# Optimization experiments

Measured on AMD Instinct MI355X. Metric: run time of the kernel, lower is better.

## Reference

```python
import jax, jax.numpy as jnp
import numpy as np

N_IN, N_HID, N_OUT = 2048, 4096, 1024
N_TOT = N_IN + N_HID + N_OUT
BATCH = 4096


def _structure_mask():
    # input -> {hidden, output}; hidden -> {hidden, output}; nothing feeds inputs,
    # outputs feed nothing.
    m = np.zeros((N_TOT, N_TOT), dtype=np.float32)
    m[0:N_IN, N_IN:N_TOT] = 1.0
    m[N_IN:N_IN + N_HID, N_IN:N_TOT] = 1.0
    return jnp.asarray(m)


def setup_inputs() -> dict:
    key = jax.random.key(0)
    kx, kw = jax.random.split(key)
    x = jax.random.normal(kx, (BATCH, N_IN), dtype=jnp.float32)
    weights = jax.random.normal(kw, (N_TOT, N_TOT), dtype=jnp.float32) * 0.1
    structure_mask = _structure_mask()
    return {"x": x, "weights": weights, "structure_mask": structure_mask}


def reference(x, weights, structure_mask):
    # Faithful to the torch forward: the per-neuron hidden loop reads the
    # activation vector BEFORE any hidden value is written, so every hidden
    # unit sees only [x, 0, 0]; outputs then see [x, hidden, 0].
    Wm = weights * structure_mask  # (N_TOT, N_TOT)
    B = x.shape[0]
    a0 = jnp.concatenate(
        [x, jnp.zeros((B, N_HID + N_OUT), dtype=x.dtype)], axis=1)  # (B, N_TOT)
    hidden = jax.nn.relu(a0 @ Wm[:, N_IN:N_IN + N_HID])             # (B, N_HID)
    a1 = jnp.concatenate(
        [x, hidden, jnp.zeros((B, N_OUT), dtype=x.dtype)], axis=1)  # (B, N_TOT)
    out = a1 @ Wm[:, N_IN + N_HID:]                                 # (B, N_OUT)
    return out
```

## Files before the change

kernel.cpp:

```cpp
#include <hip/hip_runtime.h>
#include <hip/hip_bf16.h>

#define N_IN  2048
#define N_HID 4096
#define N_OUT 1024
#define N_TOT 7168
#define BATCH 4096
#define LDA2  (N_IN + N_HID)
#define OUT_ELEMS ((size_t)BATCH * N_OUT)

typedef __attribute__((ext_vector_type(8))) short short8;
typedef __attribute__((ext_vector_type(4))) float f32x4;

static __device__ __forceinline__ unsigned short f2bf(float f) {
  __hip_bfloat16 h = __float2bfloat16(f);
  return __builtin_bit_cast(unsigned short, h);
}

__global__ void conv_x_kernel(const float* __restrict__ x,
                              unsigned short* __restrict__ A2) {
  int idx = blockIdx.x * 256 + threadIdx.x;
  int row = idx >> 9;
  int col = (idx & 511) << 2;
  const float4 v = *(const float4*)(x + (size_t)row * N_IN + col);
  ushort4 o;
  o.x = f2bf(v.x); o.y = f2bf(v.y); o.z = f2bf(v.z); o.w = f2bf(v.w);
  *(ushort4*)(A2 + (size_t)row * LDA2 + col) = o;
}

__global__ void conv_t_kernel(const float* __restrict__ src, int lds_,
                              unsigned short* __restrict__ dst, int ldd) {
  __shared__ float tile[32][33];
  const int t = threadIdx.x;
  const int k0 = blockIdx.y << 5, n0 = blockIdx.x << 5;
  const int r = t >> 3, c = (t & 7) << 2;
  const float4 v = *(const float4*)(src + (size_t)(k0 + r) * lds_ + n0 + c);
  tile[r][c] = v.x; tile[r][c + 1] = v.y; tile[r][c + 2] = v.z; tile[r][c + 3] = v.w;
  __syncthreads();
  ushort4 o;
  o.x = f2bf(tile[c][r]);
  o.y = f2bf(tile[c + 1][r]);
  o.z = f2bf(tile[c + 2][r]);
  o.w = f2bf(tile[c + 3][r]);
  *(ushort4*)(dst + (size_t)(n0 + r) * ldd + k0 + c) = o;
}

__global__ void add3_kernel(const float* __restrict__ P, float* __restrict__ out) {
  size_t i = ((size_t)blockIdx.x * 256 + threadIdx.x) * 4;
  float4 a = *(const float4*)(P + i);
  float4 b = *(const float4*)(P + OUT_ELEMS + i);
  float4 c = *(const float4*)(P + 2 * OUT_ELEMS + i);
  float4 o;
  o.x = (a.x + b.x) + c.x;
  o.y = (a.y + b.y) + c.y;
  o.z = (a.z + b.z) + c.z;
  o.w = (a.w + b.w) + c.w;
  *(float4*)(out + i) = o;
}

struct GemmCtx {
  int lane, wave, wy, wx, lm, quad;
  int grow, gcol;
};

static __device__ __forceinline__ void gemm_kloop(
    const unsigned short* __restrict__ Ag, int lda,
    const unsigned short* __restrict__ Bg, int ldb,
    unsigned short* As, unsigned short* Bs, const GemmCtx& cx,
    int Klen, f32x4 acc[4][4]) {
  unsigned short* Asl = As + cx.wave * 2048;
  unsigned short* Bsl = Bs + cx.wave * 2048;
  for (int ko = 0; ko < Klen; ko += 64) {
    __syncthreads();
#pragma unroll
    for (int i = 0; i < 4; ++i) {
      __builtin_amdgcn_global_load_lds(
          (const __attribute__((address_space(1))) void*)(Ag + (size_t)(8 * i) * lda + ko),
          (__attribute__((address_space(3))) void*)(Asl + i * 512), 16, 0, 0);
      __builtin_amdgcn_global_load_lds(
          (const __attribute__((address_space(1))) void*)(Bg + (size_t)(8 * i) * ldb + ko),
          (__attribute__((address_space(3))) void*)(Bsl + i * 512), 16, 0, 0);
    }
    __syncthreads();

#pragma unroll
    for (int kk = 0; kk < 2; ++kk) {
      short8 av[4], bv[4];
#pragma unroll
      for (int mt = 0; mt < 4; ++mt) {
        const int r = cx.wy * 64 + mt * 16 + cx.lm;
        av[mt] = *(const short8*)(As + r * 64 + (((kk * 4 + cx.quad) ^ (cx.lm & 7)) << 3));
      }
#pragma unroll
      for (int nt = 0; nt < 4; ++nt) {
        const int r = cx.wx * 64 + nt * 16 + cx.lm;
        bv[nt] = *(const short8*)(Bs + r * 64 + (((kk * 4 + cx.quad) ^ (cx.lm & 7)) << 3));
      }
#pragma unroll
      for (int mt = 0; mt < 4; ++mt)
#pragma unroll
        for (int nt = 0; nt < 4; ++nt)
          acc[mt][nt] = __builtin_amdgcn_mfma_f32_16x16x32_bf16(
              av[mt], bv[nt], acc[mt][nt], 0, 0, 0);
    }
  }
}

static __device__ __forceinline__ void epilogue_f32(
    char* smem, const GemmCtx& cx, f32x4 acc[4][4],
    float* __restrict__ C, int ldc, int row_base, int col_base, int tid) {
  float* Csf = (float*)smem;
#pragma unroll
  for (int p = 0; p < 2; ++p) {
    if (cx.wy == p) {
#pragma unroll
      for (int mt = 0; mt < 4; ++mt) {
        const int row0 = mt * 16 + cx.quad * 4;
#pragma unroll
        for (int nt = 0; nt < 4; ++nt) {
          const int col = cx.wx * 64 + nt * 16 + cx.lm;
#pragma unroll
          for (int r = 0; r < 4; ++r)
            Csf[(row0 + r) * 132 + col] = acc[mt][nt][r];
        }
      }
    }
    __syncthreads();
    const int col = (tid & 31) << 2;
#pragma unroll
    for (int i = 0; i < 8; ++i) {
      const int row = (tid >> 5) + 8 * i;
      float4 v = *(const float4*)(Csf + row * 132 + col);
      *(float4*)(C + (size_t)(row_base + p * 64 + row) * ldc + col_base + col) = v;
    }
    if (p == 0) __syncthreads();
  }
}

__global__ __launch_bounds__(256)
void gemm_fused(const unsigned short* __restrict__ A, int lda,
                const unsigned short* __restrict__ Bt, int ldb,
                unsigned short* __restrict__ Hout,
                float* __restrict__ P0) {
  __shared__ __align__(16) char smem[34816];
  unsigned short* As = (unsigned short*)smem;
  unsigned short* Bs = (unsigned short*)(smem + 16384);

  const int tid = threadIdx.x;
  GemmCtx cx;
  cx.lane = tid & 63; cx.wave = tid >> 6;
  cx.wy = cx.wave >> 1; cx.wx = cx.wave & 1;
  cx.lm = cx.lane & 15; cx.quad = cx.lane >> 4;
  cx.grow = (cx.wave << 5) + (cx.lane >> 3);
  cx.gcol = ((cx.lane & 7) ^ (cx.lane >> 3)) << 3;
  const int bm = blockIdx.y, bn = blockIdx.x;

  const unsigned short* Ag = A  + (size_t)(bm * 128 + cx.grow) * lda + cx.gcol;
  const unsigned short* Bg = Bt + (size_t)(bn * 128 + cx.grow) * ldb + cx.gcol;

  f32x4 acc[4][4];
#pragma unroll
  for (int i = 0; i < 4; ++i)
#pragma unroll
    for (int j = 0; j < 4; ++j)
      acc[i][j] = (f32x4){0.f, 0.f, 0.f, 0.f};

  gemm_kloop(Ag, lda, Bg, ldb, As, Bs, cx, N_IN, acc);

  __syncthreads();

  if (bn < 32) {
    unsigned short* Cs = (unsigned short*)smem;
#pragma unroll
    for (int mt = 0; mt < 4; ++mt) {
      const int row0 = cx.wy * 64 + mt * 16 + cx.quad * 4;
#pragma unroll
      for (int nt = 0; nt < 4; ++nt) {
        const int col = cx.wx * 64 + nt * 16 + cx.lm;
#pragma unroll
        for (int r = 0; r < 4; ++r) {
          float v = acc[mt][nt][r];
          Cs[(row0 + r) * 136 + col] = f2bf(v > 0.f ? v : 0.f);
        }
      }
    }
    __syncthreads();
    const int col = (tid & 15) << 3;
#pragma unroll
    for (int i = 0; i < 8; ++i) {
      const int row = (tid >> 4) + 16 * i;
      short8 v = *(const short8*)(Cs + row * 136 + col);
      *(short8*)(Hout + (size_t)(bm * 128 + row) * LDA2 + bn * 128 + col) = v;
    }
  } else {
    epilogue_f32(smem, cx, acc, P0, N_OUT, bm * 128, (bn - 32) * 128, tid);
  }
}

__global__ __launch_bounds__(256)
void gemm_p(const unsigned short* __restrict__ A, int lda,
            const unsigned short* __restrict__ Bt, int ldb,
            float* __restrict__ P) {
  __shared__ __align__(16) char smem[34816];
  unsigned short* As = (unsigned short*)smem;
  unsigned short* Bs = (unsigned short*)(smem + 16384);

  const int tid = threadIdx.x;
  GemmCtx cx;
  cx.lane = tid & 63; cx.wave = tid >> 6;
  cx.wy = cx.wave >> 1; cx.wx = cx.wave & 1;
  cx.lm = cx.lane & 15; cx.quad = cx.lane >> 4;
  cx.grow = (cx.wave << 5) + (cx.lane >> 3);
  cx.gcol = ((cx.lane & 7) ^ (cx.lane >> 3)) << 3;
  const int bm = blockIdx.y, bn = blockIdx.x;
  const int ko0 = blockIdx.z * 2048;

  const unsigned short* Ag = A  + (size_t)(bm * 128 + cx.grow) * lda + cx.gcol + ko0;
  const unsigned short* Bg = Bt + (size_t)(bn * 128 + cx.grow) * ldb + cx.gcol + ko0;

  f32x4 acc[4][4];
#pragma unroll
  for (int i = 0; i < 4; ++i)
#pragma unroll
    for (int j = 0; j < 4; ++j)
      acc[i][j] = (f32x4){0.f, 0.f, 0.f, 0.f};

  gemm_kloop(Ag, lda, Bg, ldb, As, Bs, cx, 2048, acc);

  __syncthreads();
  epilogue_f32(smem, cx, acc, P + (size_t)blockIdx.z * OUT_ELEMS, N_OUT,
               bm * 128, bn * 128, tid);
}

extern "C" void kernel_launch(void* const* d_in, const int* in_sizes, int n_in,
                              void* d_out, int out_size, void* d_ws, size_t ws_size,
                              hipStream_t stream) {
  const float* x = (const float*)d_in[0];
  const float* W = (const float*)d_in[1];

  char* ws = (char*)d_ws;
  const size_t A2_BYTES   = (size_t)BATCH * LDA2 * 2;
  const size_t BT12_BYTES = (size_t)(N_HID + N_OUT) * N_IN * 2;
  const size_t BT3_BYTES  = (size_t)N_OUT * N_HID * 2;
  unsigned short* A2   = (unsigned short*)ws;
  unsigned short* Bt12 = (unsigned short*)(ws + A2_BYTES);
  unsigned short* Bt3  = (unsigned short*)(ws + A2_BYTES + BT12_BYTES);
  float*          P    = (float*)(ws + A2_BYTES + BT12_BYTES + BT3_BYTES);

  conv_x_kernel<<<(BATCH * N_IN / 4) / 256, 256, 0, stream>>>(x, A2);

  conv_t_kernel<<<dim3((N_HID + N_OUT) / 32, N_IN / 32), 256, 0, stream>>>(
      W + N_IN, N_TOT, Bt12, N_IN);

  conv_t_kernel<<<dim3(N_OUT / 32, N_HID / 32), 256, 0, stream>>>(
      W + (size_t)N_IN * N_TOT + N_IN + N_HID, N_TOT, Bt3, N_HID);

  gemm_fused<<<dim3((N_HID + N_OUT) / 128, BATCH / 128), 256, 0, stream>>>(
      A2, LDA2, Bt12, N_IN, A2 + N_IN, P);

  gemm_p<<<dim3(N_OUT / 128, BATCH / 128, 2), 256, 0, stream>>>(
      A2 + N_IN, LDA2, Bt3, N_HID, P + OUT_ELEMS);

  add3_kernel<<<(OUT_ELEMS / 4) / 256, 256, 0, stream>>>(P, (float*)d_out);
}
```

Measured before the change: 504.6 us.

## Use 256x256 double-buffered 8-wave GEMM tiles with split-K 4 second stage

Replaces the 128x128, 4-wave GEMM kernels with 256x256 tiles run by 512 threads. The new k-loop double-buffers A and B in LDS, issues async global-to-LDS loads interleaved with MFMA phases, and uses explicit waitcnt, barriers and setprio. The second GEMM moves from split-K 2 to split-K 4, so the final reduction now sums five partial buffers. The aim is more data reuse per tile and loads hidden behind math. In exchange the larger tiles mean fewer blocks, and the extra partials add reduction traffic.

```diff
diff --git a/kernel.cpp b/kernel.cpp
--- a/kernel.cpp
+++ b/kernel.cpp
@@ -8,6 +8,7 @@
 #define BATCH 4096
 #define LDA2  (N_IN + N_HID)
 #define OUT_ELEMS ((size_t)BATCH * N_OUT)
+#define BUF 16384
 
 typedef __attribute__((ext_vector_type(8))) short short8;
 typedef __attribute__((ext_vector_type(4))) float f32x4;
@@ -45,191 +46,236 @@
   *(ushort4*)(dst + (size_t)(n0 + r) * ldd + k0 + c) = o;
 }
 
-__global__ void add3_kernel(const float* __restrict__ P, float* __restrict__ out) {
+__global__ void add5_kernel(const float* __restrict__ P, float* __restrict__ out) {
   size_t i = ((size_t)blockIdx.x * 256 + threadIdx.x) * 4;
   float4 a = *(const float4*)(P + i);
   float4 b = *(const float4*)(P + OUT_ELEMS + i);
   float4 c = *(const float4*)(P + 2 * OUT_ELEMS + i);
+  float4 d = *(const float4*)(P + 3 * OUT_ELEMS + i);
+  float4 e = *(const float4*)(P + 4 * OUT_ELEMS + i);
   float4 o;
-  o.x = (a.x + b.x) + c.x;
-  o.y = (a.y + b.y) + c.y;
-  o.z = (a.z + b.z) + c.z;
-  o.w = (a.w + b.w) + c.w;
+  o.x = ((a.x + b.x) + (c.x + d.x)) + e.x;
+  o.y = ((a.y + b.y) + (c.y + d.y)) + e.y;
+  o.z = ((a.z + b.z) + (c.z + d.z)) + e.z;
+  o.w = ((a.w + b.w) + (c.w + d.w)) + e.w;
   *(float4*)(out + i) = o;
 }
 
-struct GemmCtx {
-  int lane, wave, wy, wx, lm, quad;
-  int grow, gcol;
+struct KCtx {
+  int wave, wm, wn, lm, quad, xr, srow, arow, brow;
 };
 
-static __device__ __forceinline__ void gemm_kloop(
-    const unsigned short* __restrict__ Ag, int lda,
-    const unsigned short* __restrict__ Bg, int ldb,
-    unsigned short* As, unsigned short* Bs, const GemmCtx& cx,
-    int Klen, f32x4 acc[4][4]) {
-  unsigned short* Asl = As + cx.wave * 2048;
-  unsigned short* Bsl = Bs + cx.wave * 2048;
-  for (int ko = 0; ko < Klen; ko += 64) {
-    __syncthreads();
-#pragma unroll
-    for (int i = 0; i < 4; ++i) {
-      __builtin_amdgcn_global_load_lds(
-          (const __attribute__((address_space(1))) void*)(Ag + (size_t)(8 * i) * lda + ko),
-          (__attribute__((address_space(3))) void*)(Asl + i * 512), 16, 0, 0);
-      __builtin_amdgcn_global_load_lds(
-          (const __attribute__((address_space(1))) void*)(Bg + (size_t)(8 * i) * ldb + ko),
-          (__attribute__((address_space(3))) void*)(Bsl + i * 512), 16, 0, 0);
+static __device__ __forceinline__ void kctx_init(KCtx& c, int tid) {
+  c.wave = tid >> 6;
+  c.wm   = c.wave >> 2;
+  c.wn   = c.wave & 3;
+  c.lm   = tid & 15;
+  c.quad = (tid & 63) >> 4;
+  c.xr   = c.lm & 7;
+  c.srow = c.wave * 16;
+  c.arow = (c.wm * 128 + c.lm) * 64;
+  c.brow = (c.wn * 64  + c.lm) * 64;
+}
+
+#define GLDS(GP, LP) __builtin_amdgcn_global_load_lds( \
+    (const __attribute__((address_space(1))) void*)(GP), \
+    (__attribute__((address_space(3))) void*)(LP), 16, 0, 0)
+
+#define STG(GBASE, LD, LBASE, H, KC) do {                                     \
+    GLDS((GBASE) + (size_t)((H)*128 + c.srow    ) * (LD) + (KC),              \
+         (LBASE) + ((H)*128 + c.srow    ) * 64);                              \
+    GLDS((GBASE) + (size_t)((H)*128 + c.srow + 8) * (LD) + (KC),              \
+         (LBASE) + ((H)*128 + c.srow + 8) * 64);                              \
+  } while (0)
+
+#define LDB(BB) do {                                                          \
+    _Pragma("unroll") for (int nt = 0; nt < 4; ++nt)                          \
+    _Pragma("unroll") for (int kk = 0; kk < 2; ++kk)                          \
+      bv[nt][kk] = *(const short8*)((BB) + c.brow + nt * 1024 +               \
+                                    (((kk * 4 + c.quad) ^ c.xr) << 3));       \
+  } while (0)
+
+#define LDA_(AB, Q) do {                                                      \
+    _Pragma("unroll") for (int j = 0; j < 2; ++j)                             \
+    _Pragma("unroll") for (int kk = 0; kk < 2; ++kk)                          \
+      av[j][kk] = *(const short8*)((AB) + c.arow + (2 * (Q) + j) * 1024 +     \
+                                   (((kk * 4 + c.quad) ^ c.xr) << 3));        \
+  } while (0)
+
+#define MM(Q) do {                                                            \
+    _Pragma("unroll") for (int kk = 0; kk < 2; ++kk)                          \
+    _Pragma("unroll") for (int j = 0; j < 2; ++j)                             \
+    _Pragma("unroll") for (int nt = 0; nt < 4; ++nt)                          \
+      acc[2 * (Q) + j][nt] = __builtin_amdgcn_mfma_f32_16x16x32_bf16(         \
+          av[j][kk], bv[nt][kk], acc[2 * (Q) + j][nt], 0, 0, 0);              \
+  } while (0)
+
+#define BAR       __builtin_amdgcn_s_barrier()
+#define WAITLGKM  asm volatile("s_waitcnt lgkmcnt(0)" ::: "memory")
+#define WAITVM4   asm volatile("s_waitcnt vmcnt(4)" ::: "memory")
+#define WAITVM0   asm volatile("s_waitcnt vmcnt(0)" ::: "memory")
+#define PRIO1     __builtin_amdgcn_s_setprio(1)
+#define PRIO0     __builtin_amdgcn_s_setprio(0)
+
+static __device__ __forceinline__ void kloop_256(
+    const unsigned short* __restrict__ Agl,
+    const unsigned short* __restrict__ Bgl,
+    const int lda, const int ldb, const int kiters,
+    unsigned short* __restrict__ S, const KCtx& c, f32x4 acc[8][4]) {
+  unsigned short* const A0 = S;
+  unsigned short* const A1 = S + BUF;
+  unsigned short* const B0 = S + 2 * BUF;
+  unsigned short* const B1 = S + 3 * BUF;
+
+  short8 bv[4][2], av[2][2];
+
+  STG(Agl, lda, A0, 0, 0); STG(Agl, lda, A0, 1, 0);
+  STG(Bgl, ldb, B0, 0, 0); STG(Bgl, ldb, B0, 1, 0);
+  STG(Bgl, ldb, B1, 0, 64); STG(Bgl, ldb, B1, 1, 64);
+  WAITVM4;
+  BAR;
+
+#pragma unroll 1
+  for (int i = 0; i < kiters - 1; ++i) {
+    const int k1 = i * 128 + 64, k2 = i * 128 + 128, k3 = i * 128 + 192;
+    LDB(B0); LDA_(A0, 0); STG(Agl, lda, A1, 0, k1);
+    BAR; WAITLGKM; PRIO1; MM(0); PRIO0; BAR;
+    LDA_(A0, 1); STG(Agl, lda, A1, 1, k1);
+    BAR; WAITLGKM; PRIO1; MM(1); PRIO0; BAR;
+    LDA_(A0, 2); STG(Bgl, ldb, B0, 0, k2);
+    BAR; WAITLGKM; PRIO1; MM(2); PRIO0; BAR;
+    LDA_(A0, 3); STG(Bgl, ldb, B0, 1, k2);
+    WAITVM4; BAR; WAITLGKM; PRIO1; MM(3); PRIO0; BAR;
+    LDB(B1); LDA_(A1, 0); STG(Agl, lda, A0, 0, k2);
+    BAR; WAITLGKM; PRIO1; MM(0); PRIO0; BAR;
+    LDA_(A1, 1); STG(Agl, lda, A0, 1, k2);
+    BAR; WAITLGKM; PRIO1; MM(1); PRIO0; BAR;
+    LDA_(A1, 2); STG(Bgl, ldb, B1, 0, k3);
+    BAR; WAITLGKM; PRIO1; MM(2); PRIO0; BAR;
+    LDA_(A1, 3); STG(Bgl, ldb, B1, 1, k3);
+    WAITVM4; BAR; WAITLGKM; PRIO1; MM(3); PRIO0; BAR;
+  }
+  {
+    const int k1 = (kiters - 1) * 128 + 64;
+    LDB(B0); LDA_(A0, 0); STG(Agl, lda, A1, 0, k1);
+    BAR; WAITLGKM; PRIO1; MM(0); PRIO0; BAR;
+    LDA_(A0, 1); STG(Agl, lda, A1, 1, k1);
+    BAR; WAITLGKM; PRIO1; MM(1); PRIO0; BAR;
+    LDA_(A0, 2);
+    BAR; WAITLGKM; PRIO1; MM(2); PRIO0; BAR;
+    LDA_(A0, 3);
+    WAITVM0; BAR; WAITLGKM; PRIO1; MM(3); PRIO0; BAR;
+    LDB(B1); LDA_(A1, 0);
+    BAR; WAITLGKM; PRIO1; MM(0); PRIO0; BAR;
+    LDA_(A1, 1);
+    BAR; WAITLGKM; PRIO1; MM(1); PRIO0; BAR;
+    LDA_(A1, 2);
+    BAR; WAITLGKM; PRIO1; MM(2); PRIO0; BAR;
+    LDA_(A1, 3);
+    BAR; WAITLGKM; PRIO1; MM(3); PRIO0; BAR;
+  }
+}
+
+template <bool TO_BF16_RELU>
+static __device__ __forceinline__ void epi_store(
+    unsigned short* __restrict__ S, const KCtx& c, int tid, f32x4 acc[8][4],
+    void* __restrict__ Cout, int ldc, int rowb, int colb) {
+  float* Cf = (float*)S;
+#pragma unroll 1
+  for (int p = 0; p < 4; ++p) {
+    if (c.wm == (p >> 1)) {
+      const int mtb = (p & 1) * 4;
+#pragma unroll
+      for (int mt = 0; mt < 4; ++mt)
+#pragma unroll
+        for (int nt = 0; nt < 4; ++nt)
+#pragma unroll
+          for (int r = 0; r < 4; ++r)
+            Cf[(mt * 16 + c.quad * 4 + r) * 260 + c.wn * 64 + nt * 16 + c.lm] =
+                acc[mtb + mt][nt][r];
     }
     __syncthreads();
-
-#pragma unroll
-    for (int kk = 0; kk < 2; ++kk) {
-      short8 av[4], bv[4];
-#pragma unroll
-      for (int mt = 0; mt < 4; ++mt) {
-        const int r = cx.wy * 64 + mt * 16 + cx.lm;
-        av[mt] = *(const short8*)(As + r * 64 + (((kk * 4 + cx.quad) ^ (cx.lm & 7)) << 3));
-      }
-#pragma unroll
-      for (int nt = 0; nt < 4; ++nt) {
-        const int r = cx.wx * 64 + nt * 16 + cx.lm;
-        bv[nt] = *(const short8*)(Bs + r * 64 + (((kk * 4 + cx.quad) ^ (cx.lm & 7)) << 3));
-      }
-#pragma unroll
-      for (int mt = 0; mt < 4; ++mt)
-#pragma unroll
-        for (int nt = 0; nt < 4; ++nt)
-          acc[mt][nt] = __builtin_amdgcn_mfma_f32_16x16x32_bf16(
-              av[mt], bv[nt], acc[mt][nt], 0, 0, 0);
-    }
-  }
-}
-
-static __device__ __forceinline__ void epilogue_f32(
-    char* smem, const GemmCtx& cx, f32x4 acc[4][4],
-    float* __restrict__ C, int ldc, int row_base, int col_base, int tid) {
-  float* Csf = (float*)smem;
-#pragma unroll
-  for (int p = 0; p < 2; ++p) {
-    if (cx.wy == p) {
-#pragma unroll
-      for (int mt = 0; mt < 4; ++mt) {
-        const int row0 = mt * 16 + cx.quad * 4;
-#pragma unroll
-        for (int nt = 0; nt < 4; ++nt) {
-          const int col = cx.wx * 64 + nt * 16 + cx.lm;
-#pragma unroll
-          for (int r = 0; r < 4; ++r)
-            Csf[(row0 + r) * 132 + col] = acc[mt][nt][r];
-        }
+    const int c4 = (tid & 63) * 4;
+    const int r0 = tid >> 6;
+#pragma unroll
+    for (int j = 0; j < 8; ++j) {
+      const int row = r0 + 8 * j;
+      float4 v = *(const float4*)(Cf + row * 260 + c4);
+      if (TO_BF16_RELU) {
+        ushort4 o;
+        o.x = f2bf(v.x > 0.f ? v.x : 0.f);
+        o.y = f2bf(v.y > 0.f ? v.y : 0.f);
+        o.z = f2bf(v.z > 0.f ? v.z : 0.f);
+        o.w = f2bf(v.w > 0.f ? v.w : 0.f);
+        *(ushort4*)((unsigned short*)Cout +
+                    (size_t)(rowb + p * 64 + row) * ldc + colb + c4) = o;
+      } else {
+        *(float4*)((float*)Cout +
+                   (size_t)(rowb + p * 64 + row) * ldc + colb + c4) = v;
       }
     }
     __syncthreads();
-    const int col = (tid & 31) << 2;
-#pragma unroll
-    for (int i = 0; i < 8; ++i) {
-      const int row = (tid >> 5) + 8 * i;
-      float4 v = *(const float4*)(Csf + row * 132 + col);
-      *(float4*)(C + (size_t)(row_base + p * 64 + row) * ldc + col_base + col) = v;
-    }
-    if (p == 0) __syncthreads();
   }
 }
 
-__global__ __launch_bounds__(256)
-void gemm_fused(const unsigned short* __restrict__ A, int lda,
-                const unsigned short* __restrict__ Bt, int ldb,
-                unsigned short* __restrict__ Hout,
-                float* __restrict__ P0) {
-  __shared__ __align__(16) char smem[34816];
-  unsigned short* As = (unsigned short*)smem;
-  unsigned short* Bs = (unsigned short*)(smem + 16384);
-
+__global__ __launch_bounds__(512, 2)
+void gemm_fused2(const unsigned short* __restrict__ A,
+                 const unsigned short* __restrict__ Bt,
+                 unsigned short* __restrict__ Hout,
+                 float* __restrict__ P0) {
+  __shared__ __align__(16) unsigned short S[4 * BUF];
   const int tid = threadIdx.x;
-  GemmCtx cx;
-  cx.lane = tid & 63; cx.wave = tid >> 6;
-  cx.wy = cx.wave >> 1; cx.wx = cx.wave & 1;
-  cx.lm = cx.lane & 15; cx.quad = cx.lane >> 4;
-  cx.grow = (cx.wave << 5) + (cx.lane >> 3);
-  cx.gcol = ((cx.lane & 7) ^ (cx.lane >> 3)) << 3;
+  const int lane = tid & 63;
+  KCtx c; kctx_init(c, tid);
   const int bm = blockIdx.y, bn = blockIdx.x;
-
-  const unsigned short* Ag = A  + (size_t)(bm * 128 + cx.grow) * lda + cx.gcol;
-  const unsigned short* Bg = Bt + (size_t)(bn * 128 + cx.grow) * ldb + cx.gcol;
-
-  f32x4 acc[4][4];
-#pragma unroll
-  for (int i = 0; i < 4; ++i)
+  const int gcol = ((lane & 7) ^ (lane >> 3)) << 3;
+
+  const unsigned short* Agl = A  + (size_t)(bm * 256 + (lane >> 3)) * LDA2 + gcol;
+  const unsigned short* Bgl = Bt + (size_t)(bn * 256 + (lane >> 3)) * N_IN + gcol;
+
+  f32x4 acc[8][4];
+#pragma unroll
+  for (int i = 0; i < 8; ++i)
 #pragma unroll
     for (int j = 0; j < 4; ++j)
       acc[i][j] = (f32x4){0.f, 0.f, 0.f, 0.f};
 
-  gemm_kloop(Ag, lda, Bg, ldb, As, Bs, cx, N_IN, acc);
-
+  kloop_256(Agl, Bgl, LDA2, N_IN, N_IN / 128, S, c, acc);
   __syncthreads();
 
-  if (bn < 32) {
-    unsigned short* Cs = (unsigned short*)smem;
-#pragma unroll
-    for (int mt = 0; mt < 4; ++mt) {
-      const int row0 = cx.wy * 64 + mt * 16 + cx.quad * 4;
-#pragma unroll
-      for (int nt = 0; nt < 4; ++nt) {
-        const int col = cx.wx * 64 + nt * 16 + cx.lm;
-#pragma unroll
-        for (int r = 0; r < 4; ++r) {
-          float v = acc[mt][nt][r];
-          Cs[(row0 + r) * 136 + col] = f2bf(v > 0.f ? v : 0.f);
-        }
-      }
-    }
-    __syncthreads();
-    const int col = (tid & 15) << 3;
-#pragma unroll
-    for (int i = 0; i < 8; ++i) {
-      const int row = (tid >> 4) + 16 * i;
-      short8 v = *(const short8*)(Cs + row * 136 + col);
-      *(short8*)(Hout + (size_t)(bm * 128 + row) * LDA2 + bn * 128 + col) = v;
-    }
-  } else {
-    epilogue_f32(smem, cx, acc, P0, N_OUT, bm * 128, (bn - 32) * 128, tid);
-  }
-}
-
-__global__ __launch_bounds__(256)
-void gemm_p(const unsigned short* __restrict__ A, int lda,
-            const unsigned short* __restrict__ Bt, int ldb,
-            float* __restrict__ P) {
-  __shared__ __align__(16) char smem[34816];
-  unsigned short* As = (unsigned short*)smem;
-  unsigned short* Bs = (unsigned short*)(smem + 16384);
-
+  if (bn < 16)
+    epi_store<true >(S, c, tid, acc, Hout, LDA2, bm * 256, bn * 256);
+  else
+    epi_store<false>(S, c, tid, acc, P0, N_OUT, bm * 256, (bn - 16) * 256);
+}
+
+__global__ __launch_bounds__(512, 2)
+void gemm_p2(const unsigned short* __restrict__ A,
+             const unsigned short* __restrict__ Bt,
+             float* __restrict__ P) {
+  __shared__ __align__(16) unsigned short S[4 * BUF];
   const int tid = threadIdx.x;
-  GemmCtx cx;
-  cx.lane = tid & 63; cx.wave = tid >> 6;
-  cx.wy = cx.wave >> 1; cx.wx = cx.wave & 1;
-  cx.lm = cx.lane & 15; cx.quad = cx.lane >> 4;
-  cx.grow = (cx.wave << 5) + (cx.lane >> 3);
-  cx.gcol = ((cx.lane & 7) ^ (cx.lane >> 3)) << 3;
+  const int lane = tid & 63;
+  KCtx c; kctx_init(c, tid);
   const int bm = blockIdx.y, bn = blockIdx.x;
-  const int ko0 = blockIdx.z * 2048;
-
-  const unsigned short* Ag = A  + (size_t)(bm * 128 + cx.grow) * lda + cx.gcol + ko0;
-  const unsigned short* Bg = Bt + (size_t)(bn * 128 + cx.grow) * ldb + cx.gcol + ko0;
-
-  f32x4 acc[4][4];
-#pragma unroll
-  for (int i = 0; i < 4; ++i)
+  const int ko0 = blockIdx.z * 1024;
+  const int gcol = ((lane & 7) ^ (lane >> 3)) << 3;
+
+  const unsigned short* Agl = A  + (size_t)(bm * 256 + (lane >> 3)) * LDA2 + gcol + ko0;
+  const unsigned short* Bgl = Bt + (size_t)(bn * 256 + (lane >> 3)) * N_HID + gcol + ko0;
+
+  f32x4 acc[8][4];
+#pragma unroll
+  for (int i = 0; i < 8; ++i)
 #pragma unroll
     for (int j = 0; j < 4; ++j)
       acc[i][j] = (f32x4){0.f, 0.f, 0.f, 0.f};
 
-  gemm_kloop(Ag, lda, Bg, ldb, As, Bs, cx, 2048, acc);
-
+  kloop_256(Agl, Bgl, LDA2, N_HID, 1024 / 128, S, c, acc);
   __syncthreads();
-  epilogue_f32(smem, cx, acc, P + (size_t)blockIdx.z * OUT_ELEMS, N_OUT,
-               bm * 128, bn * 128, tid);
+
+  epi_store<false>(S, c, tid, acc, P + (size_t)blockIdx.z * OUT_ELEMS, N_OUT,
+                   bm * 256, bn * 256);
 }
 
 extern "C" void kernel_launch(void* const* d_in, const int* in_sizes, int n_in,
@@ -255,11 +301,11 @@
   conv_t_kernel<<<dim3(N_OUT / 32, N_HID / 32), 256, 0, stream>>>(
       W + (size_t)N_IN * N_TOT + N_IN + N_HID, N_TOT, Bt3, N_HID);
 
-  gemm_fused<<<dim3((N_HID + N_OUT) / 128, BATCH / 128), 256, 0, stream>>>(
-      A2, LDA2, Bt12, N_IN, A2 + N_IN, P);
-
-  gemm_p<<<dim3(N_OUT / 128, BATCH / 128, 2), 256, 0, stream>>>(
-      A2 + N_IN, LDA2, Bt3, N_HID, P + OUT_ELEMS);
-
-  add3_kernel<<<(OUT_ELEMS / 4) / 256, 256, 0, stream>>>(P, (float*)d_out);
-}
+  gemm_fused2<<<dim3((N_HID + N_OUT) / 256, BATCH / 256), 512, 0, stream>>>(
+      A2, Bt12, A2 + N_IN, P);
+
+  gemm_p2<<<dim3(N_OUT / 256, BATCH / 256, 4), 512, 0, stream>>>(
+      A2 + N_IN, Bt3, P + OUT_ELEMS);
+
+  add5_kernel<<<(OUT_ELEMS / 4) / 256, 256, 0, stream>>>(P, (float*)d_out);
+}
```

Result: slower. 571.3 us (+13.2%).
